# Performance work log

Measured on AMD Instinct MI355X. Metric: run time of the kernel, lower is better.

Reference implementation:

```python
import jax, jax.numpy as jnp
import numpy as np

B, S, HID = 2, 1024, 4096
N_HEADS, N_KV_HEADS = 32, 8
HEAD_DIM = HID // N_HEADS          # 128
N_REP = N_HEADS // N_KV_HEADS      # 4
ROPE_THETA = 10000.0


def setup_inputs() -> dict:
    key = jax.random.key(0)
    ks = jax.random.split(key, 5)
    scale = 0.02  # keep logits in a sane range
    return {
        "hidden_states": jax.random.normal(ks[0], (B, S, HID), dtype=jnp.float32),
        "Wq": jax.random.normal(ks[1], (HID, HID), dtype=jnp.float32) * scale,
        "Wk": jax.random.normal(ks[2], (N_KV_HEADS * HEAD_DIM, HID), dtype=jnp.float32) * scale,
        "Wv": jax.random.normal(ks[3], (N_KV_HEADS * HEAD_DIM, HID), dtype=jnp.float32) * scale,
        "Wo": jax.random.normal(ks[4], (HID, HID), dtype=jnp.float32) * scale,
    }


def _rope(x, cos, sin):
    # x: [B, H, S, D]; pairs are adjacent (view_as_complex on reshape(..., -1, 2))
    xe = x[..., 0::2]
    xo = x[..., 1::2]
    # cos/sin: [S, D/2] -> broadcast [1, 1, S, D/2]
    oe = xe * cos - xo * sin
    oo = xe * sin + xo * cos
    return jnp.stack([oe, oo], axis=-1).reshape(x.shape)


def reference(hidden_states, Wq, Wk, Wv, Wo):
    b, s, _ = hidden_states.shape
    q = (hidden_states @ Wq.T).reshape(b, s, N_HEADS, HEAD_DIM).transpose(0, 2, 1, 3)
    k = (hidden_states @ Wk.T).reshape(b, s, N_KV_HEADS, HEAD_DIM).transpose(0, 2, 1, 3)
    v = (hidden_states @ Wv.T).reshape(b, s, N_KV_HEADS, HEAD_DIM).transpose(0, 2, 1, 3)

    # RoPE (prefill: positions = arange(s))
    pos = jnp.arange(s, dtype=jnp.float32)
    inv_freq = 1.0 / (ROPE_THETA ** (jnp.arange(0, HEAD_DIM, 2, dtype=jnp.float32) / HEAD_DIM))
    freqs = pos[:, None] * inv_freq[None, :]  # [S, D/2]
    cos, sin = jnp.cos(freqs), jnp.sin(freqs)
    q = _rope(q, cos, sin)
    k = _rope(k, cos, sin)

    # GQA: repeat kv heads (repeat_kv expands each kv head n_rep times contiguously)
    k = jnp.repeat(k, N_REP, axis=1)  # [B, nH, S, D]
    v = jnp.repeat(v, N_REP, axis=1)

    scores = jnp.einsum("bhsd,bhtd->bhst", q, k) / jnp.sqrt(jnp.float32(HEAD_DIM))
    causal = jnp.tril(jnp.ones((s, s), dtype=bool))  # [S, S]
    scores = jnp.where(causal[None, None], scores, jnp.finfo(scores.dtype).min)
    attn = jax.nn.softmax(scores, axis=-1)
    out = jnp.einsum("bhst,bhtd->bhsd", attn, v)  # [B, nH, S, D]
    out = out.transpose(0, 2, 1, 3).reshape(b, s, HID)
    return out @ Wo.T
```

## Files before the change

### kernel.cpp

```cpp
#include <hip/hip_runtime.h>

typedef unsigned int u32;
typedef unsigned short u16;

#define S_LEN 1024
#define NH 32
#define NKV 8
#define DW 64
#define NEG_BIG (-1e30f)

typedef __bf16 bf16x8 __attribute__((ext_vector_type(8)));
typedef float f32x4 __attribute__((ext_vector_type(4)));

__device__ __forceinline__ u16 f2bf(float f) {
  u32 u = __builtin_bit_cast(u32, f);
  u += 0x7fffu + ((u >> 16) & 1u);
  return (u16)(u >> 16);
}
__device__ __forceinline__ float bflo(u32 u) { return __builtin_bit_cast(float, u << 16); }
__device__ __forceinline__ float bfhi(u32 u) { return __builtin_bit_cast(float, u & 0xffff0000u); }

__device__ __forceinline__ void gl_lds16(const u16* g, u32* l) {
  __builtin_amdgcn_global_load_lds(
      (__attribute__((address_space(1))) void*)const_cast<u16*>(g),
      (__attribute__((address_space(3))) void*)l, 16, 0, 0);
}

__launch_bounds__(256)
__global__ void cvt_all(const float4* __restrict__ hs, const float4* __restrict__ wq,
                        const float4* __restrict__ wk, const float4* __restrict__ wv,
                        uint4* __restrict__ hs16, uint4* __restrict__ wqkv) {
  const int b = blockIdx.x;
  const float4* src;
  uint4* dst;
  int i;
  if (b < 4096)       { i = b * 256 + threadIdx.x;           src = hs; dst = hs16; }
  else if (b < 12288) { i = (b - 4096) * 256 + threadIdx.x;  src = wq; dst = wqkv; }
  else if (b < 14336) { i = (b - 12288) * 256 + threadIdx.x; src = wk; dst = wqkv + 2097152; }
  else                { i = (b - 14336) * 256 + threadIdx.x; src = wv; dst = wqkv + 2621440; }
  float4 a = src[2 * i], c = src[2 * i + 1];
  uint4 o;
  o.x = (u32)f2bf(a.x) | ((u32)f2bf(a.y) << 16);
  o.y = (u32)f2bf(a.z) | ((u32)f2bf(a.w) << 16);
  o.z = (u32)f2bf(c.x) | ((u32)f2bf(c.y) << 16);
  o.w = (u32)f2bf(c.z) | ((u32)f2bf(c.w) << 16);
  dst[i] = o;
}

__launch_bounds__(256)
__global__ void cvt_bf16(const float4* __restrict__ in, uint4* __restrict__ out, int n8) {
  int i = blockIdx.x * 256 + threadIdx.x;
  if (i >= n8) return;
  float4 a = in[2 * i], b = in[2 * i + 1];
  uint4 o;
  o.x = (u32)f2bf(a.x) | ((u32)f2bf(a.y) << 16);
  o.y = (u32)f2bf(a.z) | ((u32)f2bf(a.w) << 16);
  o.z = (u32)f2bf(b.x) | ((u32)f2bf(b.y) << 16);
  o.w = (u32)f2bf(b.z) | ((u32)f2bf(b.w) << 16);
  out[i] = o;
}

template <int MODE>
__launch_bounds__(256)
__global__ void gemm16(const u16* __restrict__ A, const u16* __restrict__ B,
                       void* __restrict__ C0, void* __restrict__ C1,
                       void* __restrict__ C2, int M, int N, int K) {
  __shared__ u32 As[128 * 16];
  __shared__ u32 Bs[128 * 16];
  const int tid = threadIdx.x;
  const int lane = tid & 63, w = tid >> 6;
  const int wr = w >> 1, wc = w & 1;
  const int col = lane & 15, quad = lane >> 4;
  const int nwg = gridDim.x * gridDim.y;
  const int bid = blockIdx.y * gridDim.x + blockIdx.x;
  const int cpx = nwg >> 3;
  const int chn = cpx >> 3;
  const int xcd = bid & 7, q = bid >> 3;
  const int cm = xcd >> 2, cn = xcd & 3;
  const int im = q / chn, in_ = q % chn;
  const int m0 = (cm * 8 + im) * 128;
  const int n0 = (cn * chn + in_) * 128;

  const u16* ap0 = A + (size_t)(m0 + (tid >> 2)) * K + (tid & 3) * 8;
  const u16* ap1 = ap0 + (size_t)64 * K;
  const u16* bp0 = B + (size_t)(n0 + (tid >> 2)) * K + (tid & 3) * 8;
  const u16* bp1 = bp0 + (size_t)64 * K;
  u32* asd0 = &As[w * 256];
  u32* asd1 = &As[1024 + w * 256];
  u32* bsd0 = &Bs[w * 256];
  u32* bsd1 = &Bs[1024 + w * 256];

  f32x4 acc[4][4] = {};

  for (int k0 = 0; k0 < K; k0 += 32) {
    gl_lds16(ap0 + k0, asd0);
    gl_lds16(ap1 + k0, asd1);
    gl_lds16(bp0 + k0, bsd0);
    gl_lds16(bp1 + k0, bsd1);
    __syncthreads();

    bf16x8 af[4], bfr[4];
#pragma unroll
    for (int i = 0; i < 4; ++i) {
      int m = wr * 64 + i * 16 + col;
      af[i] = *reinterpret_cast<const bf16x8*>(&As[m * 16 + quad * 4]);
      int n = wc * 64 + i * 16 + col;
      bfr[i] = *reinterpret_cast<const bf16x8*>(&Bs[n * 16 + quad * 4]);
    }
#pragma unroll
    for (int i = 0; i < 4; ++i)
#pragma unroll
      for (int j = 0; j < 4; ++j)
        acc[i][j] = __builtin_amdgcn_mfma_f32_16x16x32_bf16(af[i], bfr[j], acc[i][j], 0, 0, 0);
    __syncthreads();
  }

#pragma unroll
  for (int i = 0; i < 4; ++i)
#pragma unroll
    for (int j = 0; j < 4; ++j)
#pragma unroll
      for (int r = 0; r < 4; ++r) {
        int row = m0 + wr * 64 + i * 16 + quad * 4 + r;
        int cc  = n0 + wc * 64 + j * 16 + col;
        float v = acc[i][j][r];
        if constexpr (MODE == 2) {
          if (cc < 4096)      ((u16*)C0)[(size_t)row * 4096 + cc] = f2bf(v);
          else if (cc < 5120) ((u16*)C1)[(size_t)row * 1024 + (cc - 4096)] = f2bf(v);
          else                ((u16*)C2)[(size_t)row * 1024 + (cc - 5120)] = f2bf(v);
        } else {
          ((float*)C0)[(size_t)row * N + cc] = v;
        }
      }
}

__launch_bounds__(256)
__global__ void rope_all(u32* __restrict__ Qb, u32* __restrict__ Kb) {
  int pg = blockIdx.x * 256 + threadIdx.x;
  u32* buf;
  int p, heads;
  float scale;
  if (pg < 4194304) { buf = Qb; p = pg; heads = NH; scale = 0.08838834764831845f; }
  else              { buf = Kb; p = pg - 4194304; heads = NKV; scale = 1.0f; }
  int d2 = p & 63;
  int s = (p / (64 * heads)) % S_LEN;
  float ang = (float)s * expf((float)d2 * -0.14391156831212787f);
  float sn, cs;
  sincosf(ang, &sn, &cs);
  u32 u = buf[p];
  float x0 = bflo(u), x1 = bfhi(u);
  float y0 = (x0 * cs - x1 * sn) * scale;
  float y1 = (x0 * sn + x1 * cs) * scale;
  buf[p] = (u32)f2bf(y0) | ((u32)f2bf(y1) << 16);
}

__launch_bounds__(256)
__global__ void attn_kernel(const u32* __restrict__ Qb, const u32* __restrict__ Kb,
                            const u32* __restrict__ Vb, u32* __restrict__ Ob) {
  __shared__ u32 Ks[64 * 64];
  __shared__ u32 Vt[128 * 32];
  __shared__ u16 Ps[4][16 * 64];
  const int tid = threadIdx.x, lane = tid & 63, w = tid >> 6;
  const int col = lane & 15, quad = lane >> 4;
  const int id = blockIdx.x;
  const int kh = id & 7;
  const int j2 = id >> 3;
  const int b = j2 & 1, hin = (j2 >> 1) & 3, pair = j2 >> 3;
  const int h = kh * 4 + hin;

  uint4 kpf[4], vpa[2], vpb[2];
  auto prefetch = [&](int t0) {
#pragma unroll
    for (int i = 0; i < 4; ++i) {
      int f = i * 256 + tid;
      int row = f >> 4, c4 = f & 15;
      kpf[i] = *((const uint4*)(Kb + ((size_t)((b * S_LEN + t0 + row) * NKV + kh)) * DW) + c4);
    }
#pragma unroll
    for (int i = 0; i < 2; ++i) {
      int f = i * 256 + tid;
      int kp = f & 31, c8 = f >> 5;
      size_t base0 = ((size_t)((b * S_LEN + t0 + 2 * kp) * NKV + kh)) * DW;
      vpa[i] = *((const uint4*)(Vb + base0) + c8);
      vpb[i] = *((const uint4*)(Vb + base0 + (size_t)NKV * DW) + c8);
    }
  };

  prefetch(0);

  for (int half = 0; half < 2; ++half) {
    const int jt = half ? pair : (15 - pair);
    const int q0 = jt * 64 + w * 16;

    bf16x8 qf[4];
    {
      const u32* qrow = Qb + ((size_t)((b * S_LEN + q0 + col) * NH + h)) * DW;
#pragma unroll
      for (int dc = 0; dc < 4; ++dc)
        qf[dc] = *reinterpret_cast<const bf16x8*>(qrow + dc * 16 + quad * 4);
    }

    float m_r[4], l_r[4];
    f32x4 oacc[8];
#pragma unroll
    for (int r = 0; r < 4; ++r) { m_r[r] = NEG_BIG; l_r[r] = 0.f; }
#pragma unroll
    for (int dt = 0; dt < 8; ++dt) oacc[dt] = (f32x4){0.f, 0.f, 0.f, 0.f};

    for (int tt = 0; tt <= jt; ++tt) {
      const int t0 = tt * 64;
      __syncthreads();
#pragma unroll
      for (int i = 0; i < 4; ++i) {
        int f = i * 256 + tid;
        int row = f >> 4, c4 = f & 15;
        *(uint4*)&Ks[(row * 64 + c4 * 4) ^ ((row & 7) << 2)] = kpf[i];
      }
#pragma unroll
      for (int i = 0; i < 2; ++i) {
        int f = i * 256 + tid;
        int kp = f & 31, c8 = f >> 5;
        u32 a[4] = {vpa[i].x, vpa[i].y, vpa[i].z, vpa[i].w};
        u32 bbv[4] = {vpb[i].x, vpb[i].y, vpb[i].z, vpb[i].w};
#pragma unroll
        for (int t = 0; t < 4; ++t) {
          int d0 = c8 * 8 + 2 * t, d1 = d0 + 1;
          u32 lo = (a[t] & 0xffffu) | (bbv[t] << 16);
          u32 hi = (a[t] >> 16) | (bbv[t] & 0xffff0000u);
          Vt[(d0 * 32 + kp) ^ ((d0 & 7) << 2)] = lo;
          Vt[(d1 * 32 + kp) ^ ((d1 & 7) << 2)] = hi;
        }
      }
      __syncthreads();

      if (tt < jt) prefetch(t0 + 64);
      else if (half == 0) prefetch(0);

      f32x4 sacc[4];
#pragma unroll
      for (int kt = 0; kt < 4; ++kt) sacc[kt] = (f32x4){0.f, 0.f, 0.f, 0.f};
      __builtin_amdgcn_s_setprio(1);
#pragma unroll
      for (int dc = 0; dc < 4; ++dc)
#pragma unroll
        for (int kt = 0; kt < 4; ++kt) {
          int key = kt * 16 + col;
          bf16x8 kf = *reinterpret_cast<const bf16x8*>(
              &Ks[(key * 64 + dc * 16 + quad * 4) ^ ((key & 7) << 2)]);
          sacc[kt] = __builtin_amdgcn_mfma_f32_16x16x32_bf16(qf[dc], kf, sacc[kt], 0, 0, 0);
        }
      __builtin_amdgcn_s_setprio(0);

      if (tt == jt) {
#pragma unroll
        for (int kt = 0; kt < 4; ++kt)
#pragma unroll
          for (int r = 0; r < 4; ++r) {
            int tg = t0 + kt * 16 + col;
            int qg = q0 + quad * 4 + r;
            if (tg > qg) sacc[kt][r] = NEG_BIG;
          }
      }

      float mt[4];
#pragma unroll
      for (int r = 0; r < 4; ++r)
        mt[r] = fmaxf(fmaxf(sacc[0][r], sacc[1][r]), fmaxf(sacc[2][r], sacc[3][r]));
#pragma unroll
      for (int off = 1; off < 16; off <<= 1)
#pragma unroll
        for (int r = 0; r < 4; ++r) mt[r] = fmaxf(mt[r], __shfl_xor(mt[r], off));
      float alpha[4], ps[4];
#pragma unroll
      for (int r = 0; r < 4; ++r) {
        float mn = fmaxf(m_r[r], mt[r]);
        alpha[r] = __expf(m_r[r] - mn);
        m_r[r] = mn;
        ps[r] = 0.f;
      }
#pragma unroll
      for (int kt = 0; kt < 4; ++kt)
#pragma unroll
        for (int r = 0; r < 4; ++r) {
          float p = __expf(sacc[kt][r] - m_r[r]);
          u16 pb = f2bf(p);
          int rw = quad * 4 + r;
          Ps[w][(rw * 64 + kt * 16 + col) ^ ((rw & 7) << 3)] = pb;
          ps[r] += bflo((u32)pb);
        }
#pragma unroll
      for (int off = 1; off < 16; off <<= 1)
#pragma unroll
        for (int r = 0; r < 4; ++r) ps[r] += __shfl_xor(ps[r], off);
#pragma unroll
      for (int r = 0; r < 4; ++r) l_r[r] = l_r[r] * alpha[r] + ps[r];
#pragma unroll
      for (int dt = 0; dt < 8; ++dt)
#pragma unroll
        for (int r = 0; r < 4; ++r) oacc[dt][r] *= alpha[r];

      bf16x8 pa[2];
#pragma unroll
      for (int ks = 0; ks < 2; ++ks)
        pa[ks] = *reinterpret_cast<const bf16x8*>(
            &Ps[w][(col * 64 + ks * 32 + quad * 8) ^ ((col & 7) << 3)]);
      __builtin_amdgcn_s_setprio(1);
#pragma unroll
      for (int dt = 0; dt < 8; ++dt) {
        int d = dt * 16 + col;
#pragma unroll
        for (int ks = 0; ks < 2; ++ks) {
          bf16x8 vf = *reinterpret_cast<const bf16x8*>(
              &Vt[(d * 32 + ks * 16 + quad * 4) ^ ((d & 7) << 2)]);
          oacc[dt] = __builtin_amdgcn_mfma_f32_16x16x32_bf16(pa[ks], vf, oacc[dt], 0, 0, 0);
        }
      }
      __builtin_amdgcn_s_setprio(0);
    }

    float invl[4];
#pragma unroll
    for (int r = 0; r < 4; ++r) invl[r] = 1.0f / l_r[r];
    u16* O16 = (u16*)Ob;
#pragma unroll
    for (int dt = 0; dt < 8; ++dt)
#pragma unroll
      for (int r = 0; r < 4; ++r) {
        int qg = q0 + quad * 4 + r;
        int d = dt * 16 + col;
        O16[((size_t)((b * S_LEN + qg) * NH + h)) * 128 + d] = f2bf(oacc[dt][r] * invl[r]);
      }
  }
}

extern "C" void kernel_launch(void* const* d_in, const int* in_sizes, int n_in,
                              void* d_out, int out_size, void* d_ws, size_t ws_size,
                              hipStream_t stream) {
  const float* hs = (const float*)d_in[0];
  const float* Wq = (const float*)d_in[1];
  const float* Wk = (const float*)d_in[2];
  const float* Wv = (const float*)d_in[3];
  const float* Wo = (const float*)d_in[4];

  u16* Qb   = (u16*)d_out;
  u16* hs16 = (u16*)((char*)d_out + (16u << 20));
  char* ws = (char*)d_ws;
  u16* Kb   = (u16*)ws;
  u16* Vb   = (u16*)(ws + (4u << 20));
  u16* Wqkv = (u16*)(ws + (8u << 20));
  u16* Ob   = (u16*)(ws + (8u << 20));
  u16* Wo16 = (u16*)(ws + (24u << 20));

  dim3 blk(256);
  cvt_all<<<16384, blk, 0, stream>>>((const float4*)hs, (const float4*)Wq,
                                     (const float4*)Wk, (const float4*)Wv,
                                     (uint4*)hs16, (uint4*)Wqkv);
  gemm16<2><<<dim3(48, 16), blk, 0, stream>>>(hs16, Wqkv, (void*)Qb, (void*)Kb,
                                              (void*)Vb, 2048, 6144, 4096);
  rope_all<<<20480, blk, 0, stream>>>((u32*)Qb, (u32*)Kb);
  cvt_bf16<<<8192, blk, 0, stream>>>((const float4*)Wo, (uint4*)Wo16, 2097152);
  attn_kernel<<<dim3(512), blk, 0, stream>>>((const u32*)Qb, (const u32*)Kb,
                                             (const u32*)Vb, (u32*)Ob);
  gemm16<0><<<dim3(32, 16), blk, 0, stream>>>(Ob, Wo16, d_out, nullptr, nullptr,
                                              2048, 4096, 4096);
}
```

Before: 547.1 us.

## Replace 128x128 GEMM with swizzled double-buffered 256x256 tile kernel

Both projection GEMMs now use a 512-thread block computing a 256x256 tile with a K-step of 64. Operands go through a two-stage LDS ring with an XOR swizzle and explicit vmcnt waits, so the next tile's global-to-LDS copy overlaps the MFMA work on the current one. MFMA phases are raised with s_setprio, aiming at more data reuse per LDS byte and fewer stalls. The cost is far fewer blocks (192 and 128) than the GPU has CUs, about 128KB of LDS per block, and heavier register pressure.

After: 572.7 us. +4.7%, slower.

```diff
diff --git a/kernel.cpp b/kernel.cpp
--- a/kernel.cpp
+++ b/kernel.cpp
@@ -61,69 +61,156 @@
 }
 
 template <int MODE>
-__launch_bounds__(256)
-__global__ void gemm16(const u16* __restrict__ A, const u16* __restrict__ B,
-                       void* __restrict__ C0, void* __restrict__ C1,
-                       void* __restrict__ C2, int M, int N, int K) {
-  __shared__ u32 As[128 * 16];
-  __shared__ u32 Bs[128 * 16];
+__launch_bounds__(512, 2)
+__global__ void gemm256(const u16* __restrict__ A, const u16* __restrict__ B,
+                        void* __restrict__ C0, void* __restrict__ C1,
+                        void* __restrict__ C2, int M, int N, int K) {
+  __shared__ u32 L[32768];
   const int tid = threadIdx.x;
   const int lane = tid & 63, w = tid >> 6;
-  const int wr = w >> 1, wc = w & 1;
-  const int col = lane & 15, quad = lane >> 4;
-  const int nwg = gridDim.x * gridDim.y;
-  const int bid = blockIdx.y * gridDim.x + blockIdx.x;
-  const int cpx = nwg >> 3;
-  const int chn = cpx >> 3;
+  const int wm = w >> 2, wn = w & 3;
+  const int colL = lane & 15, quad = lane >> 4;
+  const int gx = gridDim.x;
+  const int bid = blockIdx.y * gx + blockIdx.x;
+  const int CN = gx >> 2, CM = gridDim.y >> 1;
   const int xcd = bid & 7, q = bid >> 3;
   const int cm = xcd >> 2, cn = xcd & 3;
-  const int im = q / chn, in_ = q % chn;
-  const int m0 = (cm * 8 + im) * 128;
-  const int n0 = (cn * chn + in_) * 128;
-
-  const u16* ap0 = A + (size_t)(m0 + (tid >> 2)) * K + (tid & 3) * 8;
-  const u16* ap1 = ap0 + (size_t)64 * K;
-  const u16* bp0 = B + (size_t)(n0 + (tid >> 2)) * K + (tid & 3) * 8;
-  const u16* bp1 = bp0 + (size_t)64 * K;
-  u32* asd0 = &As[w * 256];
-  u32* asd1 = &As[1024 + w * 256];
-  u32* bsd0 = &Bs[w * 256];
-  u32* bsd1 = &Bs[1024 + w * 256];
-
-  f32x4 acc[4][4] = {};
-
-  for (int k0 = 0; k0 < K; k0 += 32) {
-    gl_lds16(ap0 + k0, asd0);
-    gl_lds16(ap1 + k0, asd1);
-    gl_lds16(bp0 + k0, bsd0);
-    gl_lds16(bp1 + k0, bsd1);
-    __syncthreads();
-
-    bf16x8 af[4], bfr[4];
-#pragma unroll
-    for (int i = 0; i < 4; ++i) {
-      int m = wr * 64 + i * 16 + col;
-      af[i] = *reinterpret_cast<const bf16x8*>(&As[m * 16 + quad * 4]);
-      int n = wc * 64 + i * 16 + col;
-      bfr[i] = *reinterpret_cast<const bf16x8*>(&Bs[n * 16 + quad * 4]);
-    }
+  const int m0 = (cm * CM + q / CN) * 256;
+  const int n0 = (cn * CN + q % CN) * 256;
+
+  const int srow = tid >> 3;
+  const int c8s = (tid & 7) ^ (srow & 7);
+  const u16* Asrc = A + (size_t)(m0 + srow) * K + c8s * 8;
+  const u16* Bsrc = B + (size_t)(n0 + srow) * K + c8s * 8;
+  u32* ldsw = &L[w * 256];
+
+  auto stage = [&](int kt, int c) {
+    const int ko = kt * 64;
+    u32* la = ldsw + c * 16384;
 #pragma unroll
     for (int i = 0; i < 4; ++i)
-#pragma unroll
-      for (int j = 0; j < 4; ++j)
-        acc[i][j] = __builtin_amdgcn_mfma_f32_16x16x32_bf16(af[i], bfr[j], acc[i][j], 0, 0, 0);
-    __syncthreads();
+      gl_lds16(Asrc + (size_t)i * 64 * K + ko, la + i * 2048);
+#pragma unroll
+    for (int i = 0; i < 4; ++i)
+      gl_lds16(Bsrc + (size_t)i * 64 * K + ko, la + 8192 + i * 2048);
+  };
+
+  const int qs[2] = {quad ^ (colL & 7), (quad + 4) ^ (colL & 7)};
+
+  f32x4 acc[8][4] = {};
+  bf16x8 a0[4][2], a1[4][2], bb[2][2];
+
+  const int NT = K >> 6;
+  stage(0, 0);
+  stage(1, 1);
+
+  for (int kt = 0; kt < NT; ++kt) {
+    const int c = kt & 1;
+    if (kt + 1 < NT) asm volatile("s_waitcnt vmcnt(8)" ::: "memory");
+    else             asm volatile("s_waitcnt vmcnt(0)" ::: "memory");
+    __builtin_amdgcn_s_barrier();
+    __builtin_amdgcn_sched_barrier(0);
+    const u32* la = &L[c * 16384];
+    const u32* lb = la + 8192;
+
+#pragma unroll
+    for (int f = 0; f < 4; ++f)
+#pragma unroll
+      for (int ks = 0; ks < 2; ++ks)
+        a0[f][ks] = *reinterpret_cast<const bf16x8*>(
+            &la[(wm * 128 + f * 16 + colL) * 32 + qs[ks] * 4]);
+#pragma unroll
+    for (int g = 0; g < 2; ++g)
+#pragma unroll
+      for (int ks = 0; ks < 2; ++ks)
+        bb[g][ks] = *reinterpret_cast<const bf16x8*>(
+            &lb[(wn * 64 + g * 16 + colL) * 32 + qs[ks] * 4]);
+    __builtin_amdgcn_s_setprio(1);
+#pragma unroll
+    for (int f = 0; f < 4; ++f)
+#pragma unroll
+      for (int g = 0; g < 2; ++g)
+#pragma unroll
+        for (int ks = 0; ks < 2; ++ks)
+          acc[f][g] = __builtin_amdgcn_mfma_f32_16x16x32_bf16(a0[f][ks], bb[g][ks],
+                                                              acc[f][g], 0, 0, 0);
+    __builtin_amdgcn_s_setprio(0);
+    __builtin_amdgcn_s_barrier();
+
+#pragma unroll
+    for (int f = 0; f < 4; ++f)
+#pragma unroll
+      for (int ks = 0; ks < 2; ++ks)
+        a1[f][ks] = *reinterpret_cast<const bf16x8*>(
+            &la[(wm * 128 + 64 + f * 16 + colL) * 32 + qs[ks] * 4]);
+#pragma unroll
+    for (int g = 0; g < 2; ++g)
+#pragma unroll
+      for (int ks = 0; ks < 2; ++ks)
+        bb[g][ks] = *reinterpret_cast<const bf16x8*>(
+            &lb[(wn * 64 + (2 + g) * 16 + colL) * 32 + qs[ks] * 4]);
+    __builtin_amdgcn_s_setprio(1);
+#pragma unroll
+    for (int f = 0; f < 4; ++f)
+#pragma unroll
+      for (int g = 0; g < 2; ++g)
+#pragma unroll
+        for (int ks = 0; ks < 2; ++ks)
+          acc[f][2 + g] = __builtin_amdgcn_mfma_f32_16x16x32_bf16(a0[f][ks], bb[g][ks],
+                                                                  acc[f][2 + g], 0, 0, 0);
+    __builtin_amdgcn_s_setprio(0);
+    __builtin_amdgcn_s_barrier();
+
+#pragma unroll
+    for (int g = 0; g < 2; ++g)
+#pragma unroll
+      for (int ks = 0; ks < 2; ++ks)
+        bb[g][ks] = *reinterpret_cast<const bf16x8*>(
+            &lb[(wn * 64 + g * 16 + colL) * 32 + qs[ks] * 4]);
+    __builtin_amdgcn_s_setprio(1);
+#pragma unroll
+    for (int f = 0; f < 4; ++f)
+#pragma unroll
+      for (int g = 0; g < 2; ++g)
+#pragma unroll
+        for (int ks = 0; ks < 2; ++ks)
+          acc[4 + f][g] = __builtin_amdgcn_mfma_f32_16x16x32_bf16(a1[f][ks], bb[g][ks],
+                                                                  acc[4 + f][g], 0, 0, 0);
+    __builtin_amdgcn_s_setprio(0);
+    __builtin_amdgcn_s_barrier();
+
+#pragma unroll
+    for (int g = 0; g < 2; ++g)
+#pragma unroll
+      for (int ks = 0; ks < 2; ++ks)
+        bb[g][ks] = *reinterpret_cast<const bf16x8*>(
+            &lb[(wn * 64 + (2 + g) * 16 + colL) * 32 + qs[ks] * 4]);
+    __builtin_amdgcn_s_setprio(1);
+#pragma unroll
+    for (int f = 0; f < 4; ++f)
+#pragma unroll
+      for (int g = 0; g < 2; ++g)
+#pragma unroll
+        for (int ks = 0; ks < 2; ++ks)
+          acc[4 + f][2 + g] = __builtin_amdgcn_mfma_f32_16x16x32_bf16(a1[f][ks], bb[g][ks],
+                                                                      acc[4 + f][2 + g], 0, 0, 0);
+    __builtin_amdgcn_s_setprio(0);
+
+    __builtin_amdgcn_sched_barrier(0);
+    __builtin_amdgcn_s_barrier();
+    __builtin_amdgcn_sched_barrier(0);
+    if (kt + 2 < NT) stage(kt + 2, c);
   }
 
 #pragma unroll
-  for (int i = 0; i < 4; ++i)
-#pragma unroll
-    for (int j = 0; j < 4; ++j)
+  for (int fm = 0; fm < 8; ++fm)
+#pragma unroll
+    for (int fn = 0; fn < 4; ++fn)
 #pragma unroll
       for (int r = 0; r < 4; ++r) {
-        int row = m0 + wr * 64 + i * 16 + quad * 4 + r;
-        int cc  = n0 + wc * 64 + j * 16 + col;
-        float v = acc[i][j][r];
+        int row = m0 + wm * 128 + fm * 16 + quad * 4 + r;
+        int cc  = n0 + wn * 64 + fn * 16 + colL;
+        float v = acc[fm][fn][r];
         if constexpr (MODE == 2) {
           if (cc < 4096)      ((u16*)C0)[(size_t)row * 4096 + cc] = f2bf(v);
           else if (cc < 5120) ((u16*)C1)[(size_t)row * 1024 + (cc - 4096)] = f2bf(v);
@@ -355,12 +442,12 @@
   cvt_all<<<16384, blk, 0, stream>>>((const float4*)hs, (const float4*)Wq,
                                      (const float4*)Wk, (const float4*)Wv,
                                      (uint4*)hs16, (uint4*)Wqkv);
-  gemm16<2><<<dim3(48, 16), blk, 0, stream>>>(hs16, Wqkv, (void*)Qb, (void*)Kb,
-                                              (void*)Vb, 2048, 6144, 4096);
+  gemm256<2><<<dim3(24, 8), dim3(512), 0, stream>>>(hs16, Wqkv, (void*)Qb, (void*)Kb,
+                                                    (void*)Vb, 2048, 6144, 4096);
   rope_all<<<20480, blk, 0, stream>>>((u32*)Qb, (u32*)Kb);
   cvt_bf16<<<8192, blk, 0, stream>>>((const float4*)Wo, (uint4*)Wo16, 2097152);
   attn_kernel<<<dim3(512), blk, 0, stream>>>((const u32*)Qb, (const u32*)Kb,
                                              (const u32*)Vb, (u32*)Ob);
-  gemm16<0><<<dim3(32, 16), blk, 0, stream>>>(Ob, Wo16, d_out, nullptr, nullptr,
-                                              2048, 4096, 4096);
-}
+  gemm256<0><<<dim3(16, 8), dim3(512), 0, stream>>>(Ob, Wo16, d_out, nullptr, nullptr,
+                                                    2048, 4096, 4096);
+}
```
